# Kernel optimization log

Hardware: AMD Instinct MI355X
Metric: run time of the kernel (lower is better)

## Reference

```python
import jax, jax.numpy as jnp
import numpy as np

# AccumulateKnn with distances == 1.0 everywhere and n_moments=0:
# weight w = exp(-distance) = exp(-1); output = concat(mean_k(w*f), max_k(w*f))
_W = float(np.exp(-1.0))


def _accumulate_knn(features, idx):
    # features: [N, F], idx: [N, K] -> [N, 2F]
    g = features[idx]                      # [N, K, F] neighbour gather
    mean = jnp.mean(g, axis=1) * _W        # [N, F]
    mx = jnp.max(g, axis=1) * _W           # [N, F]
    return jnp.concatenate([mean, mx], axis=-1)


def setup_inputs() -> dict:
    key = jax.random.key(0)
    k1, k2, k3, k4 = jax.random.split(key, 4)
    N, K, F = 200000, 32, 64
    x = jax.random.normal(k1, (N, F), dtype=jnp.float32)
    neighbour_indices = jax.random.randint(k2, (N, K), 0, N, dtype=jnp.int64)
    W0 = jax.random.normal(k3, (F, 64), dtype=jnp.float32) * (1.0 / np.sqrt(F))
    b0 = jnp.zeros((64,), dtype=jnp.float32)
    W1 = jax.random.normal(k4, (128, 64), dtype=jnp.float32) * (1.0 / np.sqrt(128))
    b1 = jnp.zeros((64,), dtype=jnp.float32)
    return {"x": x, "neighbour_indices": neighbour_indices,
            "W0": W0, "b0": b0, "W1": W1, "b1": b1}


def reference(x, neighbour_indices, W0, b0, W1, b1):
    allfeat = []
    feats = x
    for (W, b) in ((W0, b0), (W1, b1)):
        f = jax.nn.relu(feats @ W + b)            # dense + ReLU, [N, F_i]
        coll = _accumulate_knn(f, neighbour_indices)  # [N, 2*F_i]
        # subtract tiled self features: tile(f,[1,2]) == concat([f,f],-1)
        out = coll - jnp.concatenate([f, f], axis=-1)
        allfeat.append(out)
        feats = out
    return jnp.concatenate(allfeat + [x], axis=-1)  # [N, 128+128+64]
```

## Files before the change

### kernel.cpp

```cpp
#include <hip/hip_runtime.h>
#include <hip/hip_bf16.h>

typedef __hip_bfloat16 bf16;

__device__ __forceinline__ float us2f(unsigned short u) {
  union { unsigned int ui; float f; } cv; cv.ui = ((unsigned int)u) << 16; return cv.f;
}
__device__ __forceinline__ unsigned short f2us(float f) {
  union { float f; unsigned int u; } cv; cv.f = f;
  unsigned int u = cv.u;
  return (unsigned short)((u + 0x7fffu + ((u >> 16) & 1u)) >> 16);
}
__device__ __forceinline__ float lo2f(unsigned int u) {
  union { unsigned int ui; float f; } cv; cv.ui = u << 16; return cv.f;
}
__device__ __forceinline__ float hi2f(unsigned int u) {
  union { unsigned int ui; float f; } cv; cv.ui = u & 0xffff0000u; return cv.f;
}

#define WEXP 0.36787944117144233f

template<int KDIM>
__global__ __launch_bounds__(256) void dense_relu_kernel(
    const float* __restrict__ in, int in_stride,
    const float* __restrict__ W, const float* __restrict__ b,
    bf16* __restrict__ fout, float* __restrict__ xcopy, int n)
{
  __shared__ float Ws[KDIM][68];
  __shared__ float Xs[32][KDIM + 1];
  const int tx = threadIdx.x;
  const int row0 = blockIdx.x * 32;

  for (int t = tx; t < KDIM * 16; t += 256) {
    float4 w4 = ((const float4*)W)[t];
    int k = t >> 4, c4 = (t & 15) * 4;
    Ws[k][c4 + 0] = w4.x; Ws[k][c4 + 1] = w4.y; Ws[k][c4 + 2] = w4.z; Ws[k][c4 + 3] = w4.w;
  }

  constexpr int CH = KDIM / 4;
  for (int t = tx; t < 32 * CH; t += 256) {
    int rr = t / CH, kc = t - rr * CH;
    int row = row0 + rr;
    float4 f4 = make_float4(0.f, 0.f, 0.f, 0.f);
    if (row < n)
      f4 = *(const float4*)(in + (size_t)row * in_stride + kc * 4);
    Xs[rr][kc * 4 + 0] = f4.x; Xs[rr][kc * 4 + 1] = f4.y;
    Xs[rr][kc * 4 + 2] = f4.z; Xs[rr][kc * 4 + 3] = f4.w;
    if (xcopy != nullptr && row < n)
      *(float4*)(xcopy + (size_t)row * 320 + kc * 4) = f4;
  }
  __syncthreads();

  const int c = tx & 15;
  const int r = tx >> 4;
  float acc0[4] = {0.f, 0.f, 0.f, 0.f};
  float acc1[4] = {0.f, 0.f, 0.f, 0.f};
#pragma unroll 8
  for (int k = 0; k < KDIM; ++k) {
    const float4 w4 = *(const float4*)&Ws[k][c * 4];
    const float x0 = Xs[2 * r][k];
    const float x1 = Xs[2 * r + 1][k];
    acc0[0] += x0 * w4.x; acc0[1] += x0 * w4.y; acc0[2] += x0 * w4.z; acc0[3] += x0 * w4.w;
    acc1[0] += x1 * w4.x; acc1[1] += x1 * w4.y; acc1[2] += x1 * w4.z; acc1[3] += x1 * w4.w;
  }

  const float4 bb = *(const float4*)&b[c * 4];

  int row = row0 + 2 * r;
  if (row < n) {
    ushort4 o;
    o.x = f2us(fmaxf(acc0[0] + bb.x, 0.f));
    o.y = f2us(fmaxf(acc0[1] + bb.y, 0.f));
    o.z = f2us(fmaxf(acc0[2] + bb.z, 0.f));
    o.w = f2us(fmaxf(acc0[3] + bb.w, 0.f));
    *(ushort4*)((unsigned short*)fout + (size_t)row * 64 + c * 4) = o;
  }
  row = row0 + 2 * r + 1;
  if (row < n) {
    ushort4 o;
    o.x = f2us(fmaxf(acc1[0] + bb.x, 0.f));
    o.y = f2us(fmaxf(acc1[1] + bb.y, 0.f));
    o.z = f2us(fmaxf(acc1[2] + bb.z, 0.f));
    o.w = f2us(fmaxf(acc1[3] + bb.w, 0.f));
    *(ushort4*)((unsigned short*)fout + (size_t)row * 64 + c * 4) = o;
  }
}

__global__ __launch_bounds__(256) void accum_kernel(
    const bf16* __restrict__ f,
    const int* __restrict__ idx,
    float* __restrict__ out,
    int n)
{
  const int wid = threadIdx.x >> 6;
  const int lane = threadIdx.x & 63;
  const int i = blockIdx.x * 4 + wid;
  if (i >= n) return;

  int iv = 0;
  if (lane < 32) iv = idx[(size_t)i * 32 + lane];

  const int L = lane & 7;
  const int srcbase = (lane >> 3) << 2;

  float s[8], m[8];
#pragma unroll
  for (int j = 0; j < 8; ++j) { s[j] = 0.f; m[j] = -3.4e38f; }

  const char* fb = (const char*)f;
#pragma unroll
  for (int t = 0; t < 4; ++t) {
    const int nk = __shfl(iv, srcbase + t);
    const unsigned off = (((unsigned)nk) << 7) + ((unsigned)L << 4);
    const uint4 d = *(const uint4*)(fb + off);
    float v;
    v = lo2f(d.x); s[0] += v; m[0] = fmaxf(m[0], v);
    v = hi2f(d.x); s[1] += v; m[1] = fmaxf(m[1], v);
    v = lo2f(d.y); s[2] += v; m[2] = fmaxf(m[2], v);
    v = hi2f(d.y); s[3] += v; m[3] = fmaxf(m[3], v);
    v = lo2f(d.z); s[4] += v; m[4] = fmaxf(m[4], v);
    v = hi2f(d.z); s[5] += v; m[5] = fmaxf(m[5], v);
    v = lo2f(d.w); s[6] += v; m[6] = fmaxf(m[6], v);
    v = hi2f(d.w); s[7] += v; m[7] = fmaxf(m[7], v);
  }

#pragma unroll
  for (int off = 8; off <= 32; off <<= 1) {
#pragma unroll
    for (int j = 0; j < 8; ++j) {
      s[j] += __shfl_xor(s[j], off);
      m[j] = fmaxf(m[j], __shfl_xor(m[j], off));
    }
  }

  const uint4 sd = *(const uint4*)(fb + (((unsigned)i) << 7) + ((unsigned)L << 4));
  float self[8];
  self[0] = lo2f(sd.x); self[1] = hi2f(sd.x);
  self[2] = lo2f(sd.y); self[3] = hi2f(sd.y);
  self[4] = lo2f(sd.z); self[5] = hi2f(sd.z);
  self[6] = lo2f(sd.w); self[7] = hi2f(sd.w);

  const float cmean = WEXP / 32.0f;
  const int o = lane >> 3;
  float* orow = out + (size_t)i * 320;
  if (o == 0) {
    float4 a, bq;
    a.x = s[0] * cmean - self[0]; a.y = s[1] * cmean - self[1];
    a.z = s[2] * cmean - self[2]; a.w = s[3] * cmean - self[3];
    bq.x = s[4] * cmean - self[4]; bq.y = s[5] * cmean - self[5];
    bq.z = s[6] * cmean - self[6]; bq.w = s[7] * cmean - self[7];
    *(float4*)(orow + 8 * L) = a;
    *(float4*)(orow + 8 * L + 4) = bq;
  } else if (o == 1) {
    float4 a, bq;
    a.x = m[0] * WEXP - self[0]; a.y = m[1] * WEXP - self[1];
    a.z = m[2] * WEXP - self[2]; a.w = m[3] * WEXP - self[3];
    bq.x = m[4] * WEXP - self[4]; bq.y = m[5] * WEXP - self[5];
    bq.z = m[6] * WEXP - self[6]; bq.w = m[7] * WEXP - self[7];
    *(float4*)(orow + 64 + 8 * L) = a;
    *(float4*)(orow + 64 + 8 * L + 4) = bq;
  }
}

extern "C" void kernel_launch(void* const* d_in, const int* in_sizes, int n_in,
                              void* d_out, int out_size, void* d_ws, size_t ws_size,
                              hipStream_t stream) {
  const float* x  = (const float*)d_in[0];
  const int* idx  = (const int*)d_in[1];
  const float* W0 = (const float*)d_in[2];
  const float* b0 = (const float*)d_in[3];
  const float* W1 = (const float*)d_in[4];
  const float* b1 = (const float*)d_in[5];
  float* out = (float*)d_out;
  const int n = in_sizes[0] / 64;

  bf16* fbuf = (bf16*)d_ws;

  const int dblocks = (n + 31) / 32;
  const int ablocks = (n + 3) / 4;

  dense_relu_kernel<64><<<dblocks, 256, 0, stream>>>(x, 64, W0, b0, fbuf, out + 256, n);
  accum_kernel<<<ablocks, 256, 0, stream>>>(fbuf, idx, out, n);
  dense_relu_kernel<128><<<dblocks, 256, 0, stream>>>(out, 320, W1, b1, fbuf, nullptr, n);
  accum_kernel<<<ablocks, 256, 0, stream>>>(fbuf, idx, out + 128, n);
}
```

Baseline: 603.6 us.

## Compute dense layers with bf16 MFMA using hi/lo split of activations

Replaces the scalar FP32 dense+ReLU kernel with one that runs 16x16x32 bf16 MFMA instructions. Weights are transposed into shared memory as bf16. Activations are split into hi and lo bf16 parts to keep them close to fp32 accuracy, while the weights get only a single bf16 rounding. The output is now written as scattered 2-byte stores instead of vector stores, and weight precision drops, which risks accuracy.

```diff
diff --git a/kernel.cpp b/kernel.cpp
--- a/kernel.cpp
+++ b/kernel.cpp
@@ -2,6 +2,8 @@
 #include <hip/hip_bf16.h>
 
 typedef __hip_bfloat16 bf16;
+typedef __attribute__((ext_vector_type(8))) short short8;
+typedef __attribute__((ext_vector_type(4))) float f32x4;
 
 __device__ __forceinline__ float us2f(unsigned short u) {
   union { unsigned int ui; float f; } cv; cv.ui = ((unsigned int)u) << 16; return cv.f;
@@ -21,68 +23,70 @@
 #define WEXP 0.36787944117144233f
 
 template<int KDIM>
-__global__ __launch_bounds__(256) void dense_relu_kernel(
+__global__ __launch_bounds__(256) void dense_mfma_kernel(
     const float* __restrict__ in, int in_stride,
     const float* __restrict__ W, const float* __restrict__ b,
     bf16* __restrict__ fout, float* __restrict__ xcopy, int n)
 {
-  __shared__ float Ws[KDIM][68];
-  __shared__ float Xs[32][KDIM + 1];
+  constexpr int WT_STRIDE = KDIM + 8;
+  __shared__ unsigned short WT[64 * WT_STRIDE];
+
   const int tx = threadIdx.x;
-  const int row0 = blockIdx.x * 32;
-
-  for (int t = tx; t < KDIM * 16; t += 256) {
-    float4 w4 = ((const float4*)W)[t];
-    int k = t >> 4, c4 = (t & 15) * 4;
-    Ws[k][c4 + 0] = w4.x; Ws[k][c4 + 1] = w4.y; Ws[k][c4 + 2] = w4.z; Ws[k][c4 + 3] = w4.w;
-  }
-
-  constexpr int CH = KDIM / 4;
-  for (int t = tx; t < 32 * CH; t += 256) {
-    int rr = t / CH, kc = t - rr * CH;
-    int row = row0 + rr;
-    float4 f4 = make_float4(0.f, 0.f, 0.f, 0.f);
-    if (row < n)
-      f4 = *(const float4*)(in + (size_t)row * in_stride + kc * 4);
-    Xs[rr][kc * 4 + 0] = f4.x; Xs[rr][kc * 4 + 1] = f4.y;
-    Xs[rr][kc * 4 + 2] = f4.z; Xs[rr][kc * 4 + 3] = f4.w;
-    if (xcopy != nullptr && row < n)
-      *(float4*)(xcopy + (size_t)row * 320 + kc * 4) = f4;
+  for (int i = tx; i < KDIM * 64; i += 256) {
+    int k = i >> 6, c = i & 63;
+    WT[c * WT_STRIDE + k] = f2us(W[i]);
   }
   __syncthreads();
 
-  const int c = tx & 15;
-  const int r = tx >> 4;
-  float acc0[4] = {0.f, 0.f, 0.f, 0.f};
-  float acc1[4] = {0.f, 0.f, 0.f, 0.f};
-#pragma unroll 8
-  for (int k = 0; k < KDIM; ++k) {
-    const float4 w4 = *(const float4*)&Ws[k][c * 4];
-    const float x0 = Xs[2 * r][k];
-    const float x1 = Xs[2 * r + 1][k];
-    acc0[0] += x0 * w4.x; acc0[1] += x0 * w4.y; acc0[2] += x0 * w4.z; acc0[3] += x0 * w4.w;
-    acc1[0] += x1 * w4.x; acc1[1] += x1 * w4.y; acc1[2] += x1 * w4.z; acc1[3] += x1 * w4.w;
+  const int wv = tx >> 6;
+  const int lane = tx & 63;
+  const int mrow = lane & 15;
+  const int kgrp = lane >> 4;
+  const int row = blockIdx.x * 64 + wv * 16 + mrow;
+
+  f32x4 acc[4] = {};
+
+#pragma unroll
+  for (int ks = 0; ks < KDIM / 32; ++ks) {
+    const int k0 = ks * 32 + kgrp * 8;
+    float4 a0 = make_float4(0.f, 0.f, 0.f, 0.f);
+    float4 a1 = make_float4(0.f, 0.f, 0.f, 0.f);
+    if (row < n) {
+      a0 = *(const float4*)(in + (size_t)row * in_stride + k0);
+      a1 = *(const float4*)(in + (size_t)row * in_stride + k0 + 4);
+    }
+    if (xcopy != nullptr && row < n) {
+      *(float4*)(xcopy + (size_t)row * 320 + k0) = a0;
+      *(float4*)(xcopy + (size_t)row * 320 + k0 + 4) = a1;
+    }
+    short8 ahi, alo;
+    const float av[8] = {a0.x, a0.y, a0.z, a0.w, a1.x, a1.y, a1.z, a1.w};
+#pragma unroll
+    for (int j = 0; j < 8; ++j) {
+      const unsigned short h = f2us(av[j]);
+      ahi[j] = (short)h;
+      alo[j] = (short)f2us(av[j] - us2f(h));
+    }
+#pragma unroll
+    for (int ct = 0; ct < 4; ++ct) {
+      const short8 bfr = *(const short8*)&WT[(ct * 16 + mrow) * WT_STRIDE + k0];
+      acc[ct] = __builtin_amdgcn_mfma_f32_16x16x32_bf16(ahi, bfr, acc[ct], 0, 0, 0);
+      acc[ct] = __builtin_amdgcn_mfma_f32_16x16x32_bf16(alo, bfr, acc[ct], 0, 0, 0);
+    }
   }
 
-  const float4 bb = *(const float4*)&b[c * 4];
-
-  int row = row0 + 2 * r;
-  if (row < n) {
-    ushort4 o;
-    o.x = f2us(fmaxf(acc0[0] + bb.x, 0.f));
-    o.y = f2us(fmaxf(acc0[1] + bb.y, 0.f));
-    o.z = f2us(fmaxf(acc0[2] + bb.z, 0.f));
-    o.w = f2us(fmaxf(acc0[3] + bb.w, 0.f));
-    *(ushort4*)((unsigned short*)fout + (size_t)row * 64 + c * 4) = o;
-  }
-  row = row0 + 2 * r + 1;
-  if (row < n) {
-    ushort4 o;
-    o.x = f2us(fmaxf(acc1[0] + bb.x, 0.f));
-    o.y = f2us(fmaxf(acc1[1] + bb.y, 0.f));
-    o.z = f2us(fmaxf(acc1[2] + bb.z, 0.f));
-    o.w = f2us(fmaxf(acc1[3] + bb.w, 0.f));
-    *(ushort4*)((unsigned short*)fout + (size_t)row * 64 + c * 4) = o;
+#pragma unroll
+  for (int ct = 0; ct < 4; ++ct) {
+    const int col = ct * 16 + mrow;
+    const float bc = b[col];
+#pragma unroll
+    for (int r = 0; r < 4; ++r) {
+      const int orow = blockIdx.x * 64 + wv * 16 + kgrp * 4 + r;
+      if (orow < n) {
+        const float v = fmaxf(acc[ct][r] + bc, 0.f);
+        ((unsigned short*)fout)[(size_t)orow * 64 + col] = f2us(v);
+      }
+    }
   }
 }
 
@@ -176,11 +180,11 @@
 
   bf16* fbuf = (bf16*)d_ws;
 
-  const int dblocks = (n + 31) / 32;
+  const int dblocks = (n + 63) / 64;
   const int ablocks = (n + 3) / 4;
 
-  dense_relu_kernel<64><<<dblocks, 256, 0, stream>>>(x, 64, W0, b0, fbuf, out + 256, n);
+  dense_mfma_kernel<64><<<dblocks, 256, 0, stream>>>(x, 64, W0, b0, fbuf, out + 256, n);
   accum_kernel<<<ablocks, 256, 0, stream>>>(fbuf, idx, out, n);
-  dense_relu_kernel<128><<<dblocks, 256, 0, stream>>>(out, 320, W1, b1, fbuf, nullptr, n);
+  dense_mfma_kernel<128><<<dblocks, 256, 0, stream>>>(out, 320, W1, b1, fbuf, nullptr, n);
   accum_kernel<<<ablocks, 256, 0, stream>>>(fbuf, idx, out + 128, n);
 }
```

Result: faster. 572.3 us (-5.2%).
